# Performance work log

Hardware: AMD Instinct MI355X
Metric: run time of the kernel (lower is better)

## Reference

```python
import jax, jax.numpy as jnp
import numpy as np

TOPK_INC = 20  # top-k vertices per mention that form a hyperedge (torch.topk(attention_a, 20))
TOPK_OUT = 2   # top-k node reps concatenated into the output (torch.topk(X_score, k=2))


def _indicator_from_rows(att, idx):
    # att: [N, N], idx: [A] int. Rows with idx == 0 are skipped, as in the original loop.
    N = att.shape[0]
    rows = att[idx]                                   # [A, N] gather of attention rows
    _, top = jax.lax.top_k(rows, TOPK_INC)            # [A, TOPK_INC]
    mask = (idx != 0).astype(att.dtype)               # [A]
    vals = jnp.broadcast_to(mask[:, None], top.shape).reshape(-1)
    # scatter-max builds the 0/1 incidence vector (multiple mentions OR together)
    return jnp.zeros((N,), att.dtype).at[top.reshape(-1)].max(vals)  # [N]


def _forward_one(h, att, a_idx, b_idx, spk, W_w, W_b, S_w, S_b):
    # h: [N, H], att: [N, N], spk: [N] (single speaker row since speak_num == 1 -> E = 3)
    a_ind = _indicator_from_rows(att, a_idx)
    b_ind = _indicator_from_rows(att, b_idx)
    Hyper0 = jnp.stack([a_ind, b_ind, spk], axis=0)   # [E, N] binary incidence
    Dv = 1.0 / jnp.sqrt(Hyper0.sum(axis=0) + 1.0)     # sqrt(inverse(diag(Dv) + I)) diagonal, [N]
    De = 1.0 / jnp.sqrt(Hyper0.sum(axis=1))           # sqrt(inverse(diag(De))) diagonal, [E]
    Hyper = Hyper0 @ att                              # [E, N]  (dropout is identity in eval)
    Hyper_att = jax.nn.softmax(Hyper, axis=-1)        # F.softmax over last dim for 2D input
    Hyper_prime = Hyper_att @ h                       # [E, H]
    w = jax.nn.softmax(Hyper_prime @ W_w.T + W_b, axis=0)[:, 0]  # [E]
    # A = diag(Dv) @ Hyper0.T @ diag(w) @ diag(De) @ Hyper @ diag(Dv); X = A @ h.
    # Associate as M @ (K @ h) to avoid materializing the [N, N] matrix A.
    K = (w * De)[:, None] * Hyper * Dv[None, :]       # [E, N]
    M = Hyper0.T * Dv[:, None]                        # [N, E]
    X = M @ (K @ h)                                   # [N, H]
    score = (X @ S_w.T + S_b)[:, 0]                   # [N]
    _, top = jax.lax.top_k(score, TOPK_OUT)           # [2]
    return X[top].reshape(-1)                         # [2*H]


def setup_inputs() -> dict:
    key = jax.random.key(0)
    B, N, H, A = 32, 1024, 768, 8
    ks = jax.random.split(key, 8)
    inp = jax.random.normal(ks[0], (B, N, H), dtype=jnp.float32)
    word_att = jax.random.uniform(ks[1], (B, 1, N, N), dtype=jnp.float32)
    a_idx = jax.random.randint(ks[2], (B, A), 0, N)
    b_idx = jax.random.randint(ks[3], (B, A), 0, N)
    speak_num = jnp.ones((B, 1), dtype=jnp.int64 if jax.config.jax_enable_x64 else jnp.int32)
    speak_all = jax.random.randint(ks[4], (B, 3, N), 0, 2).astype(jnp.float32)
    W_w = jax.random.normal(ks[5], (1, H), dtype=jnp.float32) * (1.0 / np.sqrt(H))
    W_b = jnp.zeros((1,), dtype=jnp.float32)
    score_w = jax.random.normal(ks[6], (1, H), dtype=jnp.float32) * (1.0 / np.sqrt(H))
    score_b = jnp.zeros((1,), dtype=jnp.float32)
    return {"input": inp, "word_att": word_att, "a_idx": a_idx, "b_idx": b_idx,
            "speak_num": speak_num, "speak_all": speak_all,
            "W_w": W_w, "W_b": W_b, "score_w": score_w, "score_b": score_b}


def reference(input, word_att, a_idx, b_idx, speak_num, speak_all, W_w, W_b, score_w, score_b):
    # speak_num is all ones by construction -> exactly one speaker hyperedge per sample (E = 3)
    att = word_att[:, 0]           # [B, N, N]
    spk = speak_all[:, 0]          # [B, N]
    f = jax.vmap(_forward_one, in_axes=(0, 0, 0, 0, 0, None, None, None, None))
    return f(input, att, a_idx, b_idx, spk, W_w, W_b, score_w, score_b)  # [B, 2*H]
```

## Files before the change

### kernel.cpp

```cpp
#include <hip/hip_runtime.h>
#include <math.h>

#define B_ 32
#define N_ 1024
#define H_ 768
#define A_ 8
#define TOPK_ 20
#define CH_ 32
#define CMAX_ 1280

__device__ __forceinline__ float wsum(float x) {
#pragma unroll
    for (int off = 32; off > 0; off >>= 1) x += __shfl_xor(x, off);
    return x;
}

__global__ __launch_bounds__(1024) void k1_ind(
    const float* __restrict__ att, const int* __restrict__ a_idx,
    const int* __restrict__ b_idx, const float* __restrict__ speak_all,
    float* __restrict__ aind, float* __restrict__ bind,
    float* __restrict__ Dv, float* __restrict__ De,
    float4* __restrict__ comp, int* __restrict__ npadArr)
{
    const int b = blockIdx.x;
    const int tid = threadIdx.x;
    const int w = tid >> 6, lane = tid & 63;
    __shared__ float s_ind[2][N_];
    __shared__ float s_red[3][16];
    __shared__ int wcnt[16];
    __shared__ int woff[17];

    s_ind[0][tid] = 0.f;
    s_ind[1][tid] = 0.f;
    __syncthreads();

    const int which = w >> 3;
    const int r = w & 7;
    const int idx = which ? b_idx[b * A_ + r] : a_idx[b * A_ + r];
    if (idx != 0) {
        const float* row = att + ((size_t)b * N_ + idx) * N_;
        float v[16];
#pragma unroll
        for (int k = 0; k < 16; ++k) v[k] = row[(k << 6) + lane];
        float* dst = s_ind[which];
        for (int t2 = 0; t2 < TOPK_; ++t2) {
            float bv = v[0]; int bk = 0;
#pragma unroll
            for (int k = 1; k < 16; ++k)
                if (v[k] > bv) { bv = v[k]; bk = k; }
            int bc = (bk << 6) + lane;
#pragma unroll
            for (int off = 32; off > 0; off >>= 1) {
                float ov = __shfl_xor(bv, off);
                int oc = __shfl_xor(bc, off);
                if (ov > bv || (ov == bv && oc < bc)) { bv = ov; bc = oc; }
            }
            if (lane == 0) dst[bc] = 1.f;
            if (lane == (bc & 63)) v[bc >> 6] = -INFINITY;
        }
    }
    __syncthreads();

    const float sa = s_ind[0][tid], sb = s_ind[1][tid];
    const float ss = speak_all[(size_t)b * 3 * N_ + tid];
    aind[b * N_ + tid] = sa;
    bind[b * N_ + tid] = sb;
    Dv[b * N_ + tid] = 1.f / sqrtf(sa + sb + ss + 1.f);

    float p[3] = {sa, sb, ss};
#pragma unroll
    for (int e = 0; e < 3; ++e) {
        float x = wsum(p[e]);
        if (lane == 0) s_red[e][w] = x;
    }

    const bool act = (sa + sb + ss) > 0.f;
    const unsigned long long m = __ballot(act);
    const int wrank = (int)__popcll(m & ((1ull << lane) - 1ull));
    if (lane == 0) wcnt[w] = (int)__popcll(m);
    __syncthreads();
    if (tid == 0) {
        int s = 0;
        for (int i = 0; i < 16; ++i) { woff[i] = s; s += wcnt[i]; }
        woff[16] = s;
        npadArr[b] = (s + 127) & ~127;
    }
    if (tid < 3) {
        float s = 0.f;
        for (int i = 0; i < 16; ++i) s += s_red[tid][i];
        De[b * 3 + tid] = 1.f / sqrtf(s);
    }
    __syncthreads();
    const int nact = woff[16];
    const int npad = (nact + 127) & ~127;
    if (act)
        comp[(size_t)b * CMAX_ + woff[w] + wrank] = make_float4(__int_as_float(tid), sa, sb, ss);
    for (int i = nact + tid; i < npad; i += 1024)
        comp[(size_t)b * CMAX_ + i] = make_float4(__int_as_float(0), 0.f, 0.f, 0.f);
}

__global__ __launch_bounds__(256, 4) void kBC2(
    const float* __restrict__ att, const float4* __restrict__ comp,
    const int* __restrict__ npadArr, const float* __restrict__ h,
    const float* __restrict__ Dv,
    float* __restrict__ UGpart, float* __restrict__ MZ)
{
    const int b = blockIdx.y, chunk = blockIdx.x;
    const int n0 = chunk * 32;
    const int t = threadIdx.x;
    __shared__ float4 scomp[1024];
    __shared__ float scr[3328];
    __shared__ float sHy[96];
    __shared__ float sw6[192];
    __shared__ float smz[8];

    const int npad = npadArr[b];
    for (int i = t; i < npad; i += 256) scomp[i] = comp[(size_t)b * CMAX_ + i];
    __syncthreads();
    const int cx = t & 7, ig = t >> 3;
    {
        float a0x=0,a0y=0,a0z=0,a0w=0, a1x=0,a1y=0,a1z=0,a1w=0, a2x=0,a2y=0,a2z=0,a2w=0;
        const float* bb = att + (size_t)b * N_ * N_ + n0 + cx * 4;
#pragma unroll 4
        for (int i = ig; i < npad; i += 32) {
            const float4 c = scomp[i];
            const float4 v = *(const float4*)(bb + (size_t)__float_as_int(c.x) * N_);
            a0x += c.y*v.x; a0y += c.y*v.y; a0z += c.y*v.z; a0w += c.y*v.w;
            a1x += c.z*v.x; a1y += c.z*v.y; a1z += c.z*v.z; a1w += c.z*v.w;
            a2x += c.w*v.x; a2y += c.w*v.y; a2z += c.w*v.z; a2w += c.w*v.w;
        }
        __syncthreads();
        float vals[12] = {a0x,a0y,a0z,a0w, a1x,a1y,a1z,a1w, a2x,a2y,a2z,a2w};
#pragma unroll
        for (int k = 0; k < 12; ++k) scr[t * 13 + k] = vals[k];
        __syncthreads();
        for (int s2 = 16; s2 > 0; s2 >>= 1) {
            if (ig < s2) {
#pragma unroll
                for (int k = 0; k < 12; ++k)
                    scr[t * 13 + k] += scr[(t + s2 * 8) * 13 + k];
            }
            __syncthreads();
        }
        if (ig == 0) {
#pragma unroll
            for (int e = 0; e < 3; ++e)
#pragma unroll
                for (int j = 0; j < 4; ++j)
                    sHy[e * 32 + cx * 4 + j] = scr[t * 13 + e * 4 + j];
        }
    }
    __syncthreads();

    const int wv = t >> 6, lane = t & 63;
    if (wv < 3) {
        const float val = (lane < 32) ? sHy[wv * 32 + lane] : -INFINITY;
        float m = val;
#pragma unroll
        for (int off = 32; off > 0; off >>= 1) m = fmaxf(m, __shfl_xor(m, off));
        float z = (lane < 32) ? __expf(val - m) : 0.f;
        z = wsum(z);
        if (lane == 0) { smz[wv] = m; smz[4 + wv] = z; }
    }
    __syncthreads();
    if (t < 96) {
        const int e = t >> 5, r = t & 31;
        const float Hv = sHy[e * 32 + r];
        sw6[e * 32 + r] = __expf(Hv - smz[e]);
        sw6[96 + e * 32 + r] = Hv * Dv[b * N_ + n0 + r];
    }
    if (t < 8) MZ[(size_t)(b * CH_ + chunk) * 8 + t] = (t < 4) ? smz[t] : smz[t];
    __syncthreads();

    if (t < 192) {
        float u00=0,u01=0,u02=0,u03=0, u10=0,u11=0,u12=0,u13=0, u20=0,u21=0,u22=0,u23=0;
        float g00=0,g01=0,g02=0,g03=0, g10=0,g11=0,g12=0,g13=0, g20=0,g21=0,g22=0,g23=0;
        const float* base = h + (size_t)b * N_ * H_ + (size_t)n0 * H_ + t * 4;
#pragma unroll 8
        for (int r = 0; r < 32; ++r) {
            const float4 v = *(const float4*)(base + (size_t)r * H_);
            const float w0 = sw6[r], w1 = sw6[32 + r], w2 = sw6[64 + r];
            const float g0 = sw6[96 + r], g1 = sw6[128 + r], g2 = sw6[160 + r];
            u00 += w0*v.x; u01 += w0*v.y; u02 += w0*v.z; u03 += w0*v.w;
            u10 += w1*v.x; u11 += w1*v.y; u12 += w1*v.z; u13 += w1*v.w;
            u20 += w2*v.x; u21 += w2*v.y; u22 += w2*v.z; u23 += w2*v.w;
            g00 += g0*v.x; g01 += g0*v.y; g02 += g0*v.z; g03 += g0*v.w;
            g10 += g1*v.x; g11 += g1*v.y; g12 += g1*v.z; g13 += g1*v.w;
            g20 += g2*v.x; g21 += g2*v.y; g22 += g2*v.z; g23 += g2*v.w;
        }
        float* up = UGpart + (size_t)(b * CH_ + chunk) * 6 * H_ + t * 4;
        *(float4*)(up)        = make_float4(u00,u01,u02,u03);
        *(float4*)(up + H_)   = make_float4(u10,u11,u12,u13);
        *(float4*)(up + 2*H_) = make_float4(u20,u21,u22,u23);
        *(float4*)(up + 3*H_) = make_float4(g00,g01,g02,g03);
        *(float4*)(up + 4*H_) = make_float4(g10,g11,g12,g13);
        *(float4*)(up + 5*H_) = make_float4(g20,g21,g22,g23);
    }
}

__global__ __launch_bounds__(256) void k45_fin(
    const float* __restrict__ UGpart, const float* __restrict__ MZ,
    const float* __restrict__ De, const float* __restrict__ Dv,
    const float* __restrict__ aind, const float* __restrict__ bind,
    const float* __restrict__ speak_all,
    const float* __restrict__ W_w, const float* __restrict__ W_b,
    const float* __restrict__ S_w, const float* __restrict__ S_b,
    float* __restrict__ out)
{
    const int b = blockIdx.x, tid = threadIdx.x;
    const int lane = tid & 63, wv = tid >> 6;
    __shared__ float sUG[6 * H_];
    __shared__ float sKh[3 * H_];
    __shared__ float sscore[N_];
    __shared__ float sMZ[256];
    __shared__ float sscale[CH_ * 4];
    __shared__ float siZ[4];
    __shared__ float sred[16];
    __shared__ int sidx[4];

    if (tid < CH_ * 8) sMZ[tid] = MZ[(size_t)b * CH_ * 8 + tid];
    __syncthreads();
    if (tid < 3) {
        float m = -INFINITY;
        for (int c = 0; c < CH_; ++c) m = fmaxf(m, sMZ[c * 8 + tid]);
        float Z = 0.f;
        for (int c = 0; c < CH_; ++c) {
            const float sc = __expf(sMZ[c * 8 + tid] - m);
            sscale[c * 4 + tid] = sc;
            Z += sc * sMZ[c * 8 + 4 + tid];
        }
        siZ[tid] = 1.f / Z;
    }
    __syncthreads();

    {
        const float* p = UGpart + (size_t)b * CH_ * 6 * H_;
        for (int slot = tid; slot < 1152; slot += 256) {
            const int s = slot / 192;
            const int off = slot * 4;
            float4 a0 = make_float4(0,0,0,0), a1 = make_float4(0,0,0,0);
            if (s < 3) {
#pragma unroll
                for (int c = 0; c < CH_; c += 2) {
                    const float w0 = sscale[(c+0) * 4 + s];
                    const float w1 = sscale[(c+1) * 4 + s];
                    const float4 v0 = *(const float4*)(p + (size_t)(c+0) * 6 * H_ + off);
                    const float4 v1 = *(const float4*)(p + (size_t)(c+1) * 6 * H_ + off);
                    a0.x += w0*v0.x; a0.y += w0*v0.y; a0.z += w0*v0.z; a0.w += w0*v0.w;
                    a1.x += w1*v1.x; a1.y += w1*v1.y; a1.z += w1*v1.z; a1.w += w1*v1.w;
                }
            } else {
#pragma unroll
                for (int c = 0; c < CH_; c += 2) {
                    const float4 v0 = *(const float4*)(p + (size_t)(c+0) * 6 * H_ + off);
                    const float4 v1 = *(const float4*)(p + (size_t)(c+1) * 6 * H_ + off);
                    a0.x += v0.x; a0.y += v0.y; a0.z += v0.z; a0.w += v0.w;
                    a1.x += v1.x; a1.y += v1.y; a1.z += v1.z; a1.w += v1.w;
                }
            }
            sUG[off + 0] = a0.x + a1.x;
            sUG[off + 1] = a0.y + a1.y;
            sUG[off + 2] = a0.z + a1.z;
            sUG[off + 3] = a0.w + a1.w;
        }
    }
    __syncthreads();

    const float* Ub = sUG;
    const float* Gb = sUG + 3 * H_;

    float p0 = 0.f, p1 = 0.f, p2 = 0.f;
    for (int j = tid; j < H_; j += 256) {
        const float ww = W_w[j];
        p0 += Ub[j] * ww; p1 += Ub[H_ + j] * ww; p2 += Ub[2 * H_ + j] * ww;
    }
    p0 = wsum(p0); p1 = wsum(p1); p2 = wsum(p2);
    if (lane == 0) { sred[wv * 3 + 0] = p0; sred[wv * 3 + 1] = p1; sred[wv * 3 + 2] = p2; }
    __syncthreads();
    const float wb = W_b[0];
    const float l0 = (sred[0] + sred[3] + sred[6] + sred[9])  * siZ[0] + wb;
    const float l1 = (sred[1] + sred[4] + sred[7] + sred[10]) * siZ[1] + wb;
    const float l2 = (sred[2] + sred[5] + sred[8] + sred[11]) * siZ[2] + wb;
    const float mx = fmaxf(l0, fmaxf(l1, l2));
    const float e0 = expf(l0 - mx), e1 = expf(l1 - mx), e2 = expf(l2 - mx);
    const float inv = 1.f / (e0 + e1 + e2);
    const float wd0 = e0 * inv * De[b * 3 + 0];
    const float wd1 = e1 * inv * De[b * 3 + 1];
    const float wd2 = e2 * inv * De[b * 3 + 2];
    __syncthreads();

    for (int j = tid; j < H_; j += 256) {
        sKh[j]          = wd0 * Gb[j];
        sKh[H_ + j]     = wd1 * Gb[H_ + j];
        sKh[2 * H_ + j] = wd2 * Gb[2 * H_ + j];
    }
    __syncthreads();

    float q0 = 0.f, q1 = 0.f, q2 = 0.f;
    for (int j = tid; j < H_; j += 256) {
        const float sw2 = S_w[j];
        q0 += sKh[j] * sw2; q1 += sKh[H_ + j] * sw2; q2 += sKh[2 * H_ + j] * sw2;
    }
    q0 = wsum(q0); q1 = wsum(q1); q2 = wsum(q2);
    if (lane == 0) { sred[wv * 3 + 0] = q0; sred[wv * 3 + 1] = q1; sred[wv * 3 + 2] = q2; }
    __syncthreads();
    q0 = sred[0] + sred[3] + sred[6] + sred[9];
    q1 = sred[1] + sred[4] + sred[7] + sred[10];
    q2 = sred[2] + sred[5] + sred[8] + sred[11];

    const float sb0 = S_b[0];
    const float* av = aind + b * N_;
    const float* bv2 = bind + b * N_;
    const float* dv = Dv + b * N_;
    const float* sv = speak_all + (size_t)b * 3 * N_;
    for (int n = tid; n < N_; n += 256)
        sscore[n] = dv[n] * (av[n] * q0 + bv2[n] * q1 + sv[n] * q2) + sb0;
    __syncthreads();

    int r0;
    {
        float best = -INFINITY; int bi = N_;
        for (int n = tid; n < N_; n += 256) {
            const float s = sscore[n];
            if (s > best || (s == best && n < bi)) { best = s; bi = n; }
        }
#pragma unroll
        for (int off = 32; off > 0; off >>= 1) {
            const float ov = __shfl_xor(best, off); const int oi = __shfl_xor(bi, off);
            if (ov > best || (ov == best && oi < bi)) { best = ov; bi = oi; }
        }
        if (lane == 0) { sred[wv] = best; sidx[wv] = bi; }
        __syncthreads();
        float v = -INFINITY; int i = N_;
        for (int k = 0; k < 4; ++k)
            if (sred[k] > v || (sred[k] == v && sidx[k] < i)) { v = sred[k]; i = sidx[k]; }
        r0 = i;
    }
    __syncthreads();
    int r1;
    {
        float best = -INFINITY; int bi = N_;
        for (int n = tid; n < N_; n += 256) {
            if (n == r0) continue;
            const float s = sscore[n];
            if (s > best || (s == best && n < bi)) { best = s; bi = n; }
        }
#pragma unroll
        for (int off = 32; off > 0; off >>= 1) {
            const float ov = __shfl_xor(best, off); const int oi = __shfl_xor(bi, off);
            if (ov > best || (ov == best && oi < bi)) { best = ov; bi = oi; }
        }
        if (lane == 0) { sred[wv] = best; sidx[wv] = bi; }
        __syncthreads();
        float v = -INFINITY; int i = N_;
        for (int k = 0; k < 4; ++k)
            if (sred[k] > v || (sred[k] == v && sidx[k] < i)) { v = sred[k]; i = sidx[k]; }
        r1 = i;
    }

    float* ob = out + (size_t)b * 2 * H_;
    {
        const float d = dv[r0], wa = av[r0], wbn = bv2[r0], wsv = sv[r0];
        for (int j = tid; j < H_; j += 256)
            ob[j] = d * (wa * sKh[j] + wbn * sKh[H_ + j] + wsv * sKh[2 * H_ + j]);
    }
    {
        const float d = dv[r1], wa = av[r1], wbn = bv2[r1], wsv = sv[r1];
        for (int j = tid; j < H_; j += 256)
            ob[H_ + j] = d * (wa * sKh[j] + wbn * sKh[H_ + j] + wsv * sKh[2 * H_ + j]);
    }
}

extern "C" void kernel_launch(void* const* d_in, const int* in_sizes, int n_in,
                              void* d_out, int out_size, void* d_ws, size_t ws_size,
                              hipStream_t stream)
{
    const float* h         = (const float*)d_in[0];
    const float* att       = (const float*)d_in[1];
    const int*   a_idx     = (const int*)d_in[2];
    const int*   b_idx     = (const int*)d_in[3];
    const float* speak_all = (const float*)d_in[5];
    const float* W_w       = (const float*)d_in[6];
    const float* W_b       = (const float*)d_in[7];
    const float* S_w       = (const float*)d_in[8];
    const float* S_b       = (const float*)d_in[9];
    float* out = (float*)d_out;

    float* ws      = (float*)d_ws;
    float* aind    = ws;
    float* bind    = aind + B_ * N_;
    float* Dv      = bind + B_ * N_;
    float* De      = Dv + B_ * N_;
    int*   npadArr = (int*)(De + 128);
    float4* comp   = (float4*)(De + 256);
    float* MZ      = De + 256 + B_ * CMAX_ * 4;
    float* UGpart  = MZ + B_ * CH_ * 8;

    k1_ind<<<B_, 1024, 0, stream>>>(att, a_idx, b_idx, speak_all, aind, bind,
                                    Dv, De, comp, npadArr);
    kBC2<<<dim3(CH_, B_), 256, 0, stream>>>(att, comp, npadArr, h, Dv, UGpart, MZ);
    k45_fin<<<B_, 256, 0, stream>>>(UGpart, MZ, De, Dv, aind, bind, speak_all,
                                    W_w, W_b, S_w, S_b, out);
}
```

Baseline: 80.08 us.

## Widen kBC to 384 threads with shuffle reduction, widen final kernel to 512

The gather-accumulate kernel now runs 384 threads per block. Its shared-memory tree reduction with many barriers is replaced by cross-lane shuffles plus one small shared-memory combine over 6 waves. The h-projection stage now uses all 384 threads with float2 loads instead of 192 threads with float4. The final kernel goes from 256 to 512 threads and unrolls its chunk-combine loop by 4. The aim is more parallelism and fewer synchronisations, at the cost of narrower loads and higher register pressure under the new launch bounds.

```diff
diff --git a/kernel.cpp b/kernel.cpp
--- a/kernel.cpp
+++ b/kernel.cpp
@@ -99,7 +99,7 @@
         comp[(size_t)b * CMAX_ + i] = make_float4(__int_as_float(0), 0.f, 0.f, 0.f);
 }
 
-__global__ __launch_bounds__(256, 4) void kBC2(
+__global__ __launch_bounds__(384, 6) void kBC3(
     const float* __restrict__ att, const float4* __restrict__ comp,
     const int* __restrict__ npadArr, const float* __restrict__ h,
     const float* __restrict__ Dv,
@@ -108,51 +108,53 @@
     const int b = blockIdx.y, chunk = blockIdx.x;
     const int n0 = chunk * 32;
     const int t = threadIdx.x;
+    const int wv = t >> 6, lane = t & 63;
     __shared__ float4 scomp[1024];
-    __shared__ float scr[3328];
+    __shared__ float wred[6][8][13];
     __shared__ float sHy[96];
     __shared__ float sw6[192];
     __shared__ float smz[8];
 
     const int npad = npadArr[b];
-    for (int i = t; i < npad; i += 256) scomp[i] = comp[(size_t)b * CMAX_ + i];
-    __syncthreads();
+    for (int i = t; i < npad; i += 384) scomp[i] = comp[(size_t)b * CMAX_ + i];
+    __syncthreads();
+
     const int cx = t & 7, ig = t >> 3;
     {
         float a0x=0,a0y=0,a0z=0,a0w=0, a1x=0,a1y=0,a1z=0,a1w=0, a2x=0,a2y=0,a2z=0,a2w=0;
         const float* bb = att + (size_t)b * N_ * N_ + n0 + cx * 4;
 #pragma unroll 4
-        for (int i = ig; i < npad; i += 32) {
+        for (int i = ig; i < npad; i += 48) {
             const float4 c = scomp[i];
             const float4 v = *(const float4*)(bb + (size_t)__float_as_int(c.x) * N_);
             a0x += c.y*v.x; a0y += c.y*v.y; a0z += c.y*v.z; a0w += c.y*v.w;
             a1x += c.z*v.x; a1y += c.z*v.y; a1z += c.z*v.z; a1w += c.z*v.w;
             a2x += c.w*v.x; a2y += c.w*v.y; a2z += c.w*v.z; a2w += c.w*v.w;
         }
-        __syncthreads();
-        float vals[12] = {a0x,a0y,a0z,a0w, a1x,a1y,a1z,a1w, a2x,a2y,a2z,a2w};
-#pragma unroll
-        for (int k = 0; k < 12; ++k) scr[t * 13 + k] = vals[k];
-        __syncthreads();
-        for (int s2 = 16; s2 > 0; s2 >>= 1) {
-            if (ig < s2) {
-#pragma unroll
-                for (int k = 0; k < 12; ++k)
-                    scr[t * 13 + k] += scr[(t + s2 * 8) * 13 + k];
-            }
-            __syncthreads();
-        }
-        if (ig == 0) {
-#pragma unroll
-            for (int e = 0; e < 3; ++e)
-#pragma unroll
-                for (int j = 0; j < 4; ++j)
-                    sHy[e * 32 + cx * 4 + j] = scr[t * 13 + e * 4 + j];
-        }
-    }
-    __syncthreads();
-
-    const int wv = t >> 6, lane = t & 63;
+        float a[12] = {a0x,a0y,a0z,a0w, a1x,a1y,a1z,a1w, a2x,a2y,a2z,a2w};
+#pragma unroll
+        for (int k = 0; k < 12; ++k) {
+            float x = a[k];
+            x += __shfl_xor(x, 8);
+            x += __shfl_xor(x, 16);
+            x += __shfl_xor(x, 32);
+            a[k] = x;
+        }
+        if (lane < 8) {
+#pragma unroll
+            for (int k = 0; k < 12; ++k) wred[wv][lane][k] = a[k];
+        }
+    }
+    __syncthreads();
+    if (t < 96) {
+        const int cx2 = t / 12, k = t % 12;
+        float s = 0.f;
+#pragma unroll
+        for (int w2 = 0; w2 < 6; ++w2) s += wred[w2][cx2][k];
+        sHy[(k >> 2) * 32 + cx2 * 4 + (k & 3)] = s;
+    }
+    __syncthreads();
+
     if (wv < 3) {
         const float val = (lane < 32) ? sHy[wv * 32 + lane] : -INFINITY;
         float m = val;
@@ -169,36 +171,40 @@
         sw6[e * 32 + r] = __expf(Hv - smz[e]);
         sw6[96 + e * 32 + r] = Hv * Dv[b * N_ + n0 + r];
     }
-    if (t < 8) MZ[(size_t)(b * CH_ + chunk) * 8 + t] = (t < 4) ? smz[t] : smz[t];
-    __syncthreads();
-
-    if (t < 192) {
-        float u00=0,u01=0,u02=0,u03=0, u10=0,u11=0,u12=0,u13=0, u20=0,u21=0,u22=0,u23=0;
-        float g00=0,g01=0,g02=0,g03=0, g10=0,g11=0,g12=0,g13=0, g20=0,g21=0,g22=0,g23=0;
-        const float* base = h + (size_t)b * N_ * H_ + (size_t)n0 * H_ + t * 4;
+    if (t < 3) {
+        MZ[(size_t)(b * CH_ + chunk) * 8 + t]     = smz[t];
+        MZ[(size_t)(b * CH_ + chunk) * 8 + 4 + t] = smz[4 + t];
+    }
+    __syncthreads();
+
+    {
+        float u00=0,u01=0, u10=0,u11=0, u20=0,u21=0;
+        float g00=0,g01=0, g10=0,g11=0, g20=0,g21=0;
+        const float* base = h + (size_t)b * N_ * H_ + (size_t)n0 * H_ + t * 2;
 #pragma unroll 8
         for (int r = 0; r < 32; ++r) {
-            const float4 v = *(const float4*)(base + (size_t)r * H_);
+            const float2 v = *(const float2*)(base + (size_t)r * H_);
             const float w0 = sw6[r], w1 = sw6[32 + r], w2 = sw6[64 + r];
             const float g0 = sw6[96 + r], g1 = sw6[128 + r], g2 = sw6[160 + r];
-            u00 += w0*v.x; u01 += w0*v.y; u02 += w0*v.z; u03 += w0*v.w;
-            u10 += w1*v.x; u11 += w1*v.y; u12 += w1*v.z; u13 += w1*v.w;
-            u20 += w2*v.x; u21 += w2*v.y; u22 += w2*v.z; u23 += w2*v.w;
-            g00 += g0*v.x; g01 += g0*v.y; g02 += g0*v.z; g03 += g0*v.w;
-            g10 += g1*v.x; g11 += g1*v.y; g12 += g1*v.z; g13 += g1*v.w;
-            g20 += g2*v.x; g21 += g2*v.y; g22 += g2*v.z; g23 += g2*v.w;
-        }
-        float* up = UGpart + (size_t)(b * CH_ + chunk) * 6 * H_ + t * 4;
-        *(float4*)(up)        = make_float4(u00,u01,u02,u03);
-        *(float4*)(up + H_)   = make_float4(u10,u11,u12,u13);
-        *(float4*)(up + 2*H_) = make_float4(u20,u21,u22,u23);
-        *(float4*)(up + 3*H_) = make_float4(g00,g01,g02,g03);
-        *(float4*)(up + 4*H_) = make_float4(g10,g11,g12,g13);
-        *(float4*)(up + 5*H_) = make_float4(g20,g21,g22,g23);
+            u00 += w0*v.x; u01 += w0*v.y;
+            u10 += w1*v.x; u11 += w1*v.y;
+            u20 += w2*v.x; u21 += w2*v.y;
+            g00 += g0*v.x; g01 += g0*v.y;
+            g10 += g1*v.x; g11 += g1*v.y;
+            g20 += g2*v.x; g21 += g2*v.y;
+        }
+        float* up = UGpart + (size_t)(b * CH_ + chunk) * 6 * H_ + t * 2;
+        *(float2*)(up)          = make_float2(u00, u01);
+        *(float2*)(up + H_)     = make_float2(u10, u11);
+        *(float2*)(up + 2*H_)   = make_float2(u20, u21);
+        *(float2*)(up + 3*H_)   = make_float2(g00, g01);
+        *(float2*)(up + 4*H_)   = make_float2(g10, g11);
+        *(float2*)(up + 5*H_)   = make_float2(g20, g21);
     }
 }
 
-__global__ __launch_bounds__(256) void k45_fin(
+#define K45T_ 512
+__global__ __launch_bounds__(K45T_) void k45_fin(
     const float* __restrict__ UGpart, const float* __restrict__ MZ,
     const float* __restrict__ De, const float* __restrict__ Dv,
     const float* __restrict__ aind, const float* __restrict__ bind,
@@ -215,8 +221,9 @@
     __shared__ float sMZ[256];
     __shared__ float sscale[CH_ * 4];
     __shared__ float siZ[4];
-    __shared__ float sred[16];
-    __shared__ int sidx[4];
+    __shared__ float sred[24];
+    __shared__ float sbest[8];
+    __shared__ int sidx[8];
 
     if (tid < CH_ * 8) sMZ[tid] = MZ[(size_t)b * CH_ * 8 + tid];
     __syncthreads();
@@ -235,33 +242,44 @@
 
     {
         const float* p = UGpart + (size_t)b * CH_ * 6 * H_;
-        for (int slot = tid; slot < 1152; slot += 256) {
+        for (int slot = tid; slot < 1152; slot += K45T_) {
             const int s = slot / 192;
             const int off = slot * 4;
             float4 a0 = make_float4(0,0,0,0), a1 = make_float4(0,0,0,0);
+            float4 a2 = make_float4(0,0,0,0), a3 = make_float4(0,0,0,0);
             if (s < 3) {
 #pragma unroll
-                for (int c = 0; c < CH_; c += 2) {
+                for (int c = 0; c < CH_; c += 4) {
                     const float w0 = sscale[(c+0) * 4 + s];
                     const float w1 = sscale[(c+1) * 4 + s];
+                    const float w2 = sscale[(c+2) * 4 + s];
+                    const float w3 = sscale[(c+3) * 4 + s];
                     const float4 v0 = *(const float4*)(p + (size_t)(c+0) * 6 * H_ + off);
                     const float4 v1 = *(const float4*)(p + (size_t)(c+1) * 6 * H_ + off);
+                    const float4 v2 = *(const float4*)(p + (size_t)(c+2) * 6 * H_ + off);
+                    const float4 v3 = *(const float4*)(p + (size_t)(c+3) * 6 * H_ + off);
                     a0.x += w0*v0.x; a0.y += w0*v0.y; a0.z += w0*v0.z; a0.w += w0*v0.w;
                     a1.x += w1*v1.x; a1.y += w1*v1.y; a1.z += w1*v1.z; a1.w += w1*v1.w;
+                    a2.x += w2*v2.x; a2.y += w2*v2.y; a2.z += w2*v2.z; a2.w += w2*v2.w;
+                    a3.x += w3*v3.x; a3.y += w3*v3.y; a3.z += w3*v3.z; a3.w += w3*v3.w;
                 }
             } else {
 #pragma unroll
-                for (int c = 0; c < CH_; c += 2) {
+                for (int c = 0; c < CH_; c += 4) {
                     const float4 v0 = *(const float4*)(p + (size_t)(c+0) * 6 * H_ + off);
                     const float4 v1 = *(const float4*)(p + (size_t)(c+1) * 6 * H_ + off);
+                    const float4 v2 = *(const float4*)(p + (size_t)(c+2) * 6 * H_ + off);
+                    const float4 v3 = *(const float4*)(p + (size_t)(c+3) * 6 * H_ + off);
                     a0.x += v0.x; a0.y += v0.y; a0.z += v0.z; a0.w += v0.w;
                     a1.x += v1.x; a1.y += v1.y; a1.z += v1.z; a1.w += v1.w;
+                    a2.x += v2.x; a2.y += v2.y; a2.z += v2.z; a2.w += v2.w;
+                    a3.x += v3.x; a3.y += v3.y; a3.z += v3.z; a3.w += v3.w;
                 }
             }
-            sUG[off + 0] = a0.x + a1.x;
-            sUG[off + 1] = a0.y + a1.y;
-            sUG[off + 2] = a0.z + a1.z;
-            sUG[off + 3] = a0.w + a1.w;
+            sUG[off + 0] = a0.x + a1.x + a2.x + a3.x;
+            sUG[off + 1] = a0.y + a1.y + a2.y + a3.y;
+            sUG[off + 2] = a0.z + a1.z + a2.z + a3.z;
+            sUG[off + 3] = a0.w + a1.w + a2.w + a3.w;
         }
     }
     __syncthreads();
@@ -270,17 +288,17 @@
     const float* Gb = sUG + 3 * H_;
 
     float p0 = 0.f, p1 = 0.f, p2 = 0.f;
-    for (int j = tid; j < H_; j += 256) {
+    for (int j = tid; j < H_; j += K45T_) {
         const float ww = W_w[j];
         p0 += Ub[j] * ww; p1 += Ub[H_ + j] * ww; p2 += Ub[2 * H_ + j] * ww;
     }
     p0 = wsum(p0); p1 = wsum(p1); p2 = wsum(p2);
     if (lane == 0) { sred[wv * 3 + 0] = p0; sred[wv * 3 + 1] = p1; sred[wv * 3 + 2] = p2; }
     __syncthreads();
+    float l0 = 0.f, l1 = 0.f, l2 = 0.f;
+    for (int k = 0; k < 8; ++k) { l0 += sred[k * 3]; l1 += sred[k * 3 + 1]; l2 += sred[k * 3 + 2]; }
     const float wb = W_b[0];
-    const float l0 = (sred[0] + sred[3] + sred[6] + sred[9])  * siZ[0] + wb;
-    const float l1 = (sred[1] + sred[4] + sred[7] + sred[10]) * siZ[1] + wb;
-    const float l2 = (sred[2] + sred[5] + sred[8] + sred[11]) * siZ[2] + wb;
+    l0 = l0 * siZ[0] + wb; l1 = l1 * siZ[1] + wb; l2 = l2 * siZ[2] + wb;
     const float mx = fmaxf(l0, fmaxf(l1, l2));
     const float e0 = expf(l0 - mx), e1 = expf(l1 - mx), e2 = expf(l2 - mx);
     const float inv = 1.f / (e0 + e1 + e2);
@@ -289,7 +307,7 @@
     const float wd2 = e2 * inv * De[b * 3 + 2];
     __syncthreads();
 
-    for (int j = tid; j < H_; j += 256) {
+    for (int j = tid; j < H_; j += K45T_) {
         sKh[j]          = wd0 * Gb[j];
         sKh[H_ + j]     = wd1 * Gb[H_ + j];
         sKh[2 * H_ + j] = wd2 * Gb[2 * H_ + j];
@@ -297,30 +315,29 @@
     __syncthreads();
 
     float q0 = 0.f, q1 = 0.f, q2 = 0.f;
-    for (int j = tid; j < H_; j += 256) {
+    for (int j = tid; j < H_; j += K45T_) {
         const float sw2 = S_w[j];
         q0 += sKh[j] * sw2; q1 += sKh[H_ + j] * sw2; q2 += sKh[2 * H_ + j] * sw2;
     }
     q0 = wsum(q0); q1 = wsum(q1); q2 = wsum(q2);
     if (lane == 0) { sred[wv * 3 + 0] = q0; sred[wv * 3 + 1] = q1; sred[wv * 3 + 2] = q2; }
     __syncthreads();
-    q0 = sred[0] + sred[3] + sred[6] + sred[9];
-    q1 = sred[1] + sred[4] + sred[7] + sred[10];
-    q2 = sred[2] + sred[5] + sred[8] + sred[11];
+    q0 = 0.f; q1 = 0.f; q2 = 0.f;
+    for (int k = 0; k < 8; ++k) { q0 += sred[k * 3]; q1 += sred[k * 3 + 1]; q2 += sred[k * 3 + 2]; }
 
     const float sb0 = S_b[0];
     const float* av = aind + b * N_;
     const float* bv2 = bind + b * N_;
     const float* dv = Dv + b * N_;
     const float* sv = speak_all + (size_t)b * 3 * N_;
-    for (int n = tid; n < N_; n += 256)
+    for (int n = tid; n < N_; n += K45T_)
         sscore[n] = dv[n] * (av[n] * q0 + bv2[n] * q1 + sv[n] * q2) + sb0;
     __syncthreads();
 
     int r0;
     {
         float best = -INFINITY; int bi = N_;
-        for (int n = tid; n < N_; n += 256) {
+        for (int n = tid; n < N_; n += K45T_) {
             const float s = sscore[n];
             if (s > best || (s == best && n < bi)) { best = s; bi = n; }
         }
@@ -329,18 +346,18 @@
             const float ov = __shfl_xor(best, off); const int oi = __shfl_xor(bi, off);
             if (ov > best || (ov == best && oi < bi)) { best = ov; bi = oi; }
         }
-        if (lane == 0) { sred[wv] = best; sidx[wv] = bi; }
+        if (lane == 0) { sbest[wv] = best; sidx[wv] = bi; }
         __syncthreads();
         float v = -INFINITY; int i = N_;
-        for (int k = 0; k < 4; ++k)
-            if (sred[k] > v || (sred[k] == v && sidx[k] < i)) { v = sred[k]; i = sidx[k]; }
+        for (int k = 0; k < 8; ++k)
+            if (sbest[k] > v || (sbest[k] == v && sidx[k] < i)) { v = sbest[k]; i = sidx[k]; }
         r0 = i;
     }
     __syncthreads();
     int r1;
     {
         float best = -INFINITY; int bi = N_;
-        for (int n = tid; n < N_; n += 256) {
+        for (int n = tid; n < N_; n += K45T_) {
             if (n == r0) continue;
             const float s = sscore[n];
             if (s > best || (s == best && n < bi)) { best = s; bi = n; }
@@ -350,23 +367,23 @@
             const float ov = __shfl_xor(best, off); const int oi = __shfl_xor(bi, off);
             if (ov > best || (ov == best && oi < bi)) { best = ov; bi = oi; }
         }
-        if (lane == 0) { sred[wv] = best; sidx[wv] = bi; }
+        if (lane == 0) { sbest[wv] = best; sidx[wv] = bi; }
         __syncthreads();
         float v = -INFINITY; int i = N_;
-        for (int k = 0; k < 4; ++k)
-            if (sred[k] > v || (sred[k] == v && sidx[k] < i)) { v = sred[k]; i = sidx[k]; }
+        for (int k = 0; k < 8; ++k)
+            if (sbest[k] > v || (sbest[k] == v && sidx[k] < i)) { v = sbest[k]; i = sidx[k]; }
         r1 = i;
     }
 
     float* ob = out + (size_t)b * 2 * H_;
     {
         const float d = dv[r0], wa = av[r0], wbn = bv2[r0], wsv = sv[r0];
-        for (int j = tid; j < H_; j += 256)
+        for (int j = tid; j < H_; j += K45T_)
             ob[j] = d * (wa * sKh[j] + wbn * sKh[H_ + j] + wsv * sKh[2 * H_ + j]);
     }
     {
         const float d = dv[r1], wa = av[r1], wbn = bv2[r1], wsv = sv[r1];
-        for (int j = tid; j < H_; j += 256)
+        for (int j = tid; j < H_; j += K45T_)
             ob[H_ + j] = d * (wa * sKh[j] + wbn * sKh[H_ + j] + wsv * sKh[2 * H_ + j]);
     }
 }
@@ -398,7 +415,7 @@
 
     k1_ind<<<B_, 1024, 0, stream>>>(att, a_idx, b_idx, speak_all, aind, bind,
                                     Dv, De, comp, npadArr);
-    kBC2<<<dim3(CH_, B_), 256, 0, stream>>>(att, comp, npadArr, h, Dv, UGpart, MZ);
-    k45_fin<<<B_, 256, 0, stream>>>(UGpart, MZ, De, Dv, aind, bind, speak_all,
-                                    W_w, W_b, S_w, S_b, out);
+    kBC3<<<dim3(CH_, B_), 384, 0, stream>>>(att, comp, npadArr, h, Dv, UGpart, MZ);
+    k45_fin<<<B_, K45T_, 0, stream>>>(UGpart, MZ, De, Dv, aind, bind, speak_all,
+                                      W_w, W_b, S_w, S_b, out);
 }
```

New measurement: 78.94 us. About the same (-1.4%).
